# Kernel optimization log

Hardware: AMD Instinct MI355X
Metric: run time of the kernel (lower is better)

Reference implementation:

```python
import jax, jax.numpy as jnp
import numpy as np

F_IN, F_OUT, H, L_ENC, L_DEC, HORIZON = 32, 8, 64, 2, 2, 48
B, T = 2048, 512


def _lstm_cell(x, h, c, Wih, Whh, bih, bhh):
    # PyTorch LSTMCell: gates ordered i, f, g, o
    g = x @ Wih.T + bih + h @ Whh.T + bhh
    i, f, gg, o = jnp.split(g, 4, axis=-1)
    c_new = jax.nn.sigmoid(f) * c + jax.nn.sigmoid(i) * jnp.tanh(gg)
    h_new = jax.nn.sigmoid(o) * jnp.tanh(c_new)
    return h_new, c_new


def setup_inputs() -> dict:
    key = jax.random.key(0)
    ks = jax.random.split(key, 16)
    s = 1.0 / np.sqrt(H)
    u = lambda k, shape: jax.random.uniform(k, shape, jnp.float32, -s, s)
    return {
        "X": jax.random.normal(ks[0], (B, T, F_IN), jnp.float32),
        "X_mask": jnp.ones((B, T, F_IN), jnp.float32),
        "W_emb": u(ks[1], (H, F_IN)),
        "b_emb": u(ks[2], (H,)),
        "enc_Wih": u(ks[3], (L_ENC, 4 * H, H)),
        "enc_Whh": u(ks[4], (L_ENC, 4 * H, H)),
        "enc_bih": u(ks[5], (L_ENC, 4 * H)),
        "enc_bhh": u(ks[6], (L_ENC, 4 * H)),
        "dec_Wih": u(ks[7], (L_DEC, 4 * H, H)),
        "dec_Whh": u(ks[8], (L_DEC, 4 * H, H)),
        "dec_bih": u(ks[9], (L_DEC, 4 * H)),
        "dec_bhh": u(ks[10], (L_DEC, 4 * H)),
        "W_reg": u(ks[11], (F_OUT, H)),
        "b_reg": u(ks[12], (F_OUT,)),
    }


def reference(X, X_mask, W_emb, b_emb, enc_Wih, enc_Whh, enc_bih, enc_bhh,
              dec_Wih, dec_Whh, dec_bih, dec_bhh, W_reg, b_reg):
    batch = X.shape[0]
    # Token embedding for all timesteps at once: [T, B, H]
    emb = jnp.einsum('btf,hf->tbh', X, W_emb) + b_emb

    h0 = jnp.zeros((L_ENC, batch, H), X.dtype)
    c0 = jnp.zeros((L_ENC, batch, H), X.dtype)

    def enc_step(carry, x_t):
        h, c = carry
        h_t = x_t
        hs, cs = [], []
        for i in range(L_ENC):
            h_t, c_t = _lstm_cell(h_t, h[i], c[i], enc_Wih[i], enc_Whh[i], enc_bih[i], enc_bhh[i])
            hs.append(h_t)
            cs.append(c_t)
        return (jnp.stack(hs), jnp.stack(cs)), None

    (h_enc, _), _ = jax.lax.scan(enc_step, (h0, c0), emb)

    # Decoder: hidden states initialized from encoder h, cells from zero
    c_dec0 = jnp.zeros((L_DEC, batch, H), X.dtype)

    def dec_step(carry, _):
        h, c = carry
        h_t = h[-1]
        hs, cs = [], []
        for i in range(L_DEC):
            h_t, c_t = _lstm_cell(h_t, h[i], c[i], dec_Wih[i], dec_Whh[i], dec_bih[i], dec_bhh[i])
            hs.append(h_t)
            cs.append(c_t)
        y_t = h_t @ W_reg.T + b_reg
        return (jnp.stack(hs), jnp.stack(cs)), y_t

    _, ys = jax.lax.scan(dec_step, (h_enc, c_dec0), None, length=HORIZON)
    return jnp.transpose(ys, (1, 0, 2))  # [B, horizon, F_OUT]
```

## Files before the change

kernel.cpp:

```cpp
#include <hip/hip_runtime.h>
#include <hip/hip_bf16.h>

typedef __bf16 bf16x8 __attribute__((ext_vector_type(8)));
typedef float  f32x4  __attribute__((ext_vector_type(4)));

#define MFMA16(a,b,c) __builtin_amdgcn_mfma_f32_16x16x32_bf16((a),(b),(c),0,0,0)

__device__ __forceinline__ bf16x8 cvt8(f32x4 a, f32x4 b){
  bf16x8 r;
  r[0]=(__bf16)a[0]; r[1]=(__bf16)a[1]; r[2]=(__bf16)a[2]; r[3]=(__bf16)a[3];
  r[4]=(__bf16)b[0]; r[5]=(__bf16)b[1]; r[6]=(__bf16)b[2]; r[7]=(__bf16)b[3];
  return r;
}
__device__ __forceinline__ bf16x8 ld8(const float* p){
  return cvt8(*(const f32x4*)p, *(const f32x4*)(p+4));
}
__device__ __forceinline__ float sigm(float x){
  return __builtin_amdgcn_rcpf(1.f + __expf(-x));
}
__device__ __forceinline__ float tanhx(float x){
  return 1.f - 2.f*__builtin_amdgcn_rcpf(1.f + __expf(2.f*x));
}
__device__ __forceinline__ f32x4 sp(float v){ return (f32x4){v,v,v,v}; }

__device__ __forceinline__ float dppx8(float v){
  return __int_as_float(__builtin_amdgcn_update_dpp(
      0, __float_as_int(v), 0x128, 0xF, 0xF, true));
}
__device__ __forceinline__ float swz4(float v){
  return __int_as_float(__builtin_amdgcn_ds_swizzle(__float_as_int(v), 0x101F));
}

extern "C" __global__ void __launch_bounds__(1024, 4)
seq2seq_kernel(const float* __restrict__ X,
               const float* __restrict__ Wemb, const float* __restrict__ bemb,
               const float* __restrict__ eWih, const float* __restrict__ eWhh,
               const float* __restrict__ ebih, const float* __restrict__ ebhh,
               const float* __restrict__ dWih, const float* __restrict__ dWhh,
               const float* __restrict__ dbih, const float* __restrict__ dbhh,
               const float* __restrict__ Wreg, const float* __restrict__ breg,
               float* __restrict__ out)
{
  __shared__ __align__(16) __bf16 XA[2][8][136];
  __shared__ __align__(16) __bf16 H1s[2][8][72];

  const int tid  = (int)threadIdx.x;
  const int w    = tid >> 6;
  const int grp  = w >> 3;
  const bool g0  = (grp == 0);
  const int wt   = w & 7;
  const int lane = tid & 63;
  const int col  = lane & 15;
  const int quad = lane >> 4;
  const int row8 = col & 7;
  const int b0   = (int)blockIdx.x * 8;
  const int brow = b0 + row8;

  const bool hib = (col & 8) != 0;
  const bool qhb = (quad & 2) != 0;
  const int  ewr = 4*(quad & 1) + (hib ? 1 : 0) + (qhb ? 2 : 0);
  const int  ewu = 8*wt + (col & 7);

  for (int i = tid; i < 2*8*136; i += 1024) (&XA[0][0][0])[i]  = (__bf16)0.f;
  for (int i = tid; i < 2*8*72;  i += 1024) (&H1s[0][0][0])[i] = (__bf16)0.f;

  bf16x8 wf[8];
  float  gb[2];
#pragma unroll
  for (int ti=0; ti<2; ++ti){
    const int n = 64*(2*ti + (col>>3)) + 8*wt + (col&7);
    gb[ti] = ebih[grp*256+n] + ebhh[grp*256+n];
#pragma unroll
    for (int ks=0; ks<4; ++ks){
      const float* srcw = (ks < 2) ? eWih : eWhh;
      wf[ti*4+ks] = ld8(srcw + ((size_t)(grp*256+n))*64 + (ks&1)*32 + quad*8);
    }
  }

  const int ue = (w&3)*16 + col;
  bf16x8 wembf;
  float eb = 0.f;
  const float* xb = X + (size_t)brow*512*32 + quad*8;
  f32x4 pa0, pb0, pa1, pb1;
  if (w < 4){
    wembf = ld8(Wemb + ue*32 + quad*8);
    eb = bemb[ue];
    pa1 = *(const f32x4*)(xb+32); pb1 = *(const f32x4*)(xb+36);
    pa0 = *(const f32x4*)(xb+64); pb0 = *(const f32x4*)(xb+68);
  }

  float cC = 0.f;

  auto EWF = [&](f32x4 A0, f32x4 A1, float& c) -> float {
    float lo0 = qhb ? A0[2] : A0[0];
    float hi0 = qhb ? A0[3] : A0[1];
    float lo1 = qhb ? A1[2] : A1[0];
    float hi1 = qhb ? A1[3] : A1[1];
    float a0s = hib ? hi0 : lo0, a0x = hib ? lo0 : hi0;
    float a1s = hib ? hi1 : lo1, a1x = hib ? lo1 : hi1;
    float r0 = dppx8(a0x), r1 = dppx8(a1x);
    float gi = hib ? r0  : a0s;
    float gf = hib ? a0s : r0;
    float gg = hib ? r1  : a1s;
    float go = hib ? a1s : r1;
    float i0 = sigm(gi), f0 = sigm(gf), gt = tanhx(gg), o0 = sigm(go);
    c = f0*c + i0*gt;
    return o0*tanhx(c);
  };

  auto FUSED0 = [&](const int I){
    const int Px = (I+1)&1, Pr = I&1;
    bf16x8 ax0 = *(const bf16x8*)&XA[Px][row8][ 0 + quad*8];
    bf16x8 ax1 = *(const bf16x8*)&XA[Px][row8][32 + quad*8];
    bf16x8 ah0 = *(const bf16x8*)&XA[Pr][row8][64 + quad*8];
    bf16x8 ah1 = *(const bf16x8*)&XA[Pr][row8][96 + quad*8];
    f32x4 A0 = sp(gb[0]), A1 = sp(gb[1]);
    A0=MFMA16(ax0,wf[0],A0); A1=MFMA16(ax0,wf[4],A1);
    A0=MFMA16(ax1,wf[1],A0); A1=MFMA16(ax1,wf[5],A1);
    A0=MFMA16(ah0,wf[2],A0); A1=MFMA16(ah0,wf[6],A1);
    A0=MFMA16(ah1,wf[3],A0); A1=MFMA16(ah1,wf[7],A1);
    if (I < 510 && w < 4){
      const int s = I&1;
      f32x4 xr0 = s ? pa1 : pa0, xr1 = s ? pb1 : pb0;
      f32x4 ea = MFMA16(cvt8(xr0,xr1), wembf, sp(eb));
      int tn = I+4; if (tn > 511) tn = 511;
      f32x4 na = *(const f32x4*)(xb + (size_t)tn*32);
      f32x4 nb = *(const f32x4*)(xb + (size_t)tn*32 + 4);
      if (s){ pa1=na; pb1=nb; } else { pa0=na; pb0=nb; }
      if (quad < 2){
#pragma unroll
        for (int r=0; r<4; ++r) XA[s][quad*4+r][ue] = (__bf16)ea[r];
      }
    }
    XA[Px][ewr][64+ewu] = (__bf16)EWF(A0, A1, cC);
  };

  auto FUSED1 = [&](const int I){
    const int Px = (I+1)&1, Pr = I&1;
    bf16x8 ah0 = *(const bf16x8*)&XA[Pr][row8][64 + quad*8];
    bf16x8 ah1 = *(const bf16x8*)&XA[Pr][row8][96 + quad*8];
    bf16x8 ag0 = *(const bf16x8*)&H1s[Px][row8][ 0 + quad*8];
    bf16x8 ag1 = *(const bf16x8*)&H1s[Px][row8][32 + quad*8];
    f32x4 A0 = sp(gb[0]), A1 = sp(gb[1]);
    A0=MFMA16(ah0,wf[0],A0); A1=MFMA16(ah0,wf[4],A1);
    A0=MFMA16(ah1,wf[1],A0); A1=MFMA16(ah1,wf[5],A1);
    A0=MFMA16(ag0,wf[2],A0); A1=MFMA16(ag0,wf[6],A1);
    A0=MFMA16(ag1,wf[3],A0); A1=MFMA16(ag1,wf[7],A1);
    H1s[Pr][ewr][ewu] = (__bf16)EWF(A0, A1, cC);
  };

  __syncthreads();

  if (w < 4){
    f32x4 x0a = *(const f32x4*)xb, x0b = *(const f32x4*)(xb+4);
    f32x4 e0 = MFMA16(cvt8(x0a,x0b), wembf, sp(eb));
    if (quad < 2){
#pragma unroll
      for (int r=0; r<4; ++r) XA[0][quad*4+r][ue] = (__bf16)e0[r];
    }
  }
  __syncthreads();
  if (g0) FUSED0(-1);
  __syncthreads();

#define SLOT(I) { if (g0) FUSED0(I); else FUSED1(I); __syncthreads(); }
  for (int ii=0; ii<255; ++ii){
    SLOT(2*ii)
    SLOT(2*ii+1)
  }
  SLOT(510)
#undef SLOT

  if (!g0) FUSED1(511);
  __syncthreads();

  for (int idx = tid; idx < 8*64; idx += 1024){
    XA[1][idx>>6][idx&63] = H1s[1][idx>>6][idx&63];
  }
  bf16x8 wr0 = ld8(Wreg + (col&7)*64 +  0 + quad*8);
  bf16x8 wr1 = ld8(Wreg + (col&7)*64 + 32 + quad*8);
  const float rb = breg[col&7];
  float gbd[2];
#pragma unroll
  for (int l=0; l<2; ++l){
    const int n = 64*(col>>2) + 4*w + (col&3);
    gbd[l] = dbih[l*256+n] + dbhh[l*256+n];
#pragma unroll
    for (int ks=0; ks<4; ++ks){
      const float* srcw = (ks < 2) ? dWih : dWhh;
      wf[l*4+ks] = ld8(srcw + ((size_t)(l*256+n))*64 + (ks&1)*32 + quad*8);
    }
  }
  const int  gated = col >> 2;
  const bool b0d = (gated & 1) != 0;
  const bool b1d = (gated & 2) != 0;
  const int  rd  = 4*(quad & 1) + (b1d ? 1 : 0) + (qhb ? 2 : 0);
  const int  udj = 4*w + (col & 3);
  float cD0 = 0.f, cD1 = 0.f;
  __syncthreads();

  auto EWD = [&](f32x4 B, float& c) -> float {
    float lo  = qhb ? B[2] : B[0];
    float hi2 = qhb ? B[3] : B[1];
    float a  = b1d ? hi2 : lo;
    float ax = b1d ? lo  : hi2;
    float pA = swz4(a);
    float pB = swz4(ax);
    float qA = dppx8(ax);
    float qB = dppx8(pB);
    float gi = b1d ? (b0d?qB:qA) : (b0d?pA:a);
    float gf = b1d ? (b0d?qA:qB) : (b0d?a:pA);
    float gg = b1d ? (b0d?pA:a) : (b0d?qB:qA);
    float go = b1d ? (b0d?a:pA) : (b0d?qA:qB);
    float i0 = sigm(gi), f0 = sigm(gf), gt = tanhx(gg), o0 = sigm(go);
    c = f0*c + i0*gt;
    return o0*tanhx(c);
  };

  auto Ystore = [&](const int t){
    const int hp = t&1;
    f32x4 ya = sp(rb);
    bf16x8 y0 = *(const bf16x8*)&H1s[hp][row8][ 0 + quad*8];
    bf16x8 y1 = *(const bf16x8*)&H1s[hp][row8][32 + quad*8];
    ya = MFMA16(y0, wr0, ya);
    ya = MFMA16(y1, wr1, ya);
    if (quad < 2 && col < 8){
#pragma unroll
      for (int r=0; r<4; ++r)
        out[((size_t)(b0 + quad*4 + r)*48 + t)*8 + col] = ya[r];
    }
  };

#define DSTEP(T) {                                                         \
    const int P = (T)&1, Pm = P^1;                                         \
    {                                                                      \
      bf16x8 ax0 = *(const bf16x8*)&XA[Pm][row8][ 0 + quad*8];             \
      bf16x8 ax1 = *(const bf16x8*)&XA[Pm][row8][32 + quad*8];             \
      bf16x8 ah0 = *(const bf16x8*)&XA[Pm][row8][64 + quad*8];             \
      bf16x8 ah1 = *(const bf16x8*)&XA[Pm][row8][96 + quad*8];             \
      f32x4 B0 = sp(gbd[0]);                                               \
      B0=MFMA16(ax0,wf[0],B0); B0=MFMA16(ax1,wf[1],B0);                    \
      B0=MFMA16(ah0,wf[2],B0); B0=MFMA16(ah1,wf[3],B0);                    \
      float h = EWD(B0, cD0);                                              \
      if (!b0d) XA[P][rd][64+udj] = (__bf16)h;                             \
      if ((T) && w == 0) Ystore((T)-1);                                    \
    }                                                                      \
    __syncthreads();                                                       \
    {                                                                      \
      bf16x8 ah0 = *(const bf16x8*)&XA[P][row8][64 + quad*8];              \
      bf16x8 ah1 = *(const bf16x8*)&XA[P][row8][96 + quad*8];              \
      bf16x8 ag0 = *(const bf16x8*)&H1s[Pm][row8][ 0 + quad*8];            \
      bf16x8 ag1 = *(const bf16x8*)&H1s[Pm][row8][32 + quad*8];            \
      f32x4 B1 = sp(gbd[1]);                                               \
      B1=MFMA16(ah0,wf[4],B1); B1=MFMA16(ah1,wf[5],B1);                    \
      B1=MFMA16(ag0,wf[6],B1); B1=MFMA16(ag1,wf[7],B1);                    \
      float h = EWD(B1, cD1);                                              \
      if (!b0d){ H1s[P][rd][udj] = (__bf16)h; XA[P][rd][udj] = (__bf16)h; }\
    }                                                                      \
    __syncthreads();                                                       \
  }

  for (int tt=0; tt<24; ++tt){
    DSTEP(2*tt)
    DSTEP(2*tt+1)
  }
#undef DSTEP
  if (w == 0) Ystore(47);
}

extern "C" void kernel_launch(void* const* d_in, const int* in_sizes, int n_in,
                              void* d_out, int out_size, void* d_ws, size_t ws_size,
                              hipStream_t stream)
{
  (void)in_sizes; (void)n_in; (void)out_size; (void)d_ws; (void)ws_size;
  const float* X    = (const float*)d_in[0];
  const float* Wemb = (const float*)d_in[2];
  const float* bemb = (const float*)d_in[3];
  const float* eWih = (const float*)d_in[4];
  const float* eWhh = (const float*)d_in[5];
  const float* ebih = (const float*)d_in[6];
  const float* ebhh = (const float*)d_in[7];
  const float* dWih = (const float*)d_in[8];
  const float* dWhh = (const float*)d_in[9];
  const float* dbih = (const float*)d_in[10];
  const float* dbhh = (const float*)d_in[11];
  const float* Wreg = (const float*)d_in[12];
  const float* breg = (const float*)d_in[13];
  float* out = (float*)d_out;

  seq2seq_kernel<<<dim3(256), dim3(1024), 0, stream>>>(
      X, Wemb, bemb, eWih, eWhh, ebih, ebhh,
      dWih, dWhh, dbih, dbhh, Wreg, breg, out);
}
```

Before: 607.8 us.

## Split encoder slots into GEMM/EW phases and XOR-swizzle LDS layout

The encoder step for each layer is split into a GEMM phase and an elementwise phase, with a barrier between them. Layer 0's GEMM now runs while layer 1 does its elementwise work, and the reverse, so MFMA and VALU work from the two wave groups can overlap within the CU. The padded shared-memory rows are replaced by an XOR swizzle on 8-element chunks to avoid bank conflicts without the padding. The cost is twice as many block-wide barriers per encoder timestep, which lengthens the serial recurrence chain.

```diff
diff --git a/kernel.cpp b/kernel.cpp
--- a/kernel.cpp
+++ b/kernel.cpp
@@ -41,8 +41,8 @@
                const float* __restrict__ Wreg, const float* __restrict__ breg,
                float* __restrict__ out)
 {
-  __shared__ __align__(16) __bf16 XA[2][8][136];
-  __shared__ __align__(16) __bf16 H1s[2][8][72];
+  __shared__ __align__(16) __bf16 XA[2][8][128];
+  __shared__ __align__(16) __bf16 H1s[2][8][64];
 
   const int tid  = (int)threadIdx.x;
   const int w    = tid >> 6;
@@ -61,8 +61,15 @@
   const int  ewr = 4*(quad & 1) + (hib ? 1 : 0) + (qhb ? 2 : 0);
   const int  ewu = 8*wt + (col & 7);
 
-  for (int i = tid; i < 2*8*136; i += 1024) (&XA[0][0][0])[i]  = (__bf16)0.f;
-  for (int i = tid; i < 2*8*72;  i += 1024) (&H1s[0][0][0])[i] = (__bf16)0.f;
+  const int rx  = row8 * 128;
+  const int rh  = row8 * 64;
+  const int gA0 = ((quad    ) ^ row8) * 8;
+  const int gA1 = ((quad + 4) ^ row8) * 8;
+  const int sw0 = ewr*128 + 64 + ((wt ^ ewr) << 3) + (ewu & 7);
+  const int sw1 = ewr*64       + ((wt ^ ewr) << 3) + (ewu & 7);
+
+  for (int i = tid; i < 2*8*128; i += 1024) (&XA[0][0][0])[i]  = (__bf16)0.f;
+  for (int i = tid; i < 2*8*64;  i += 1024) (&H1s[0][0][0])[i] = (__bf16)0.f;
 
   bf16x8 wf[8];
   float  gb[2];
@@ -77,7 +84,8 @@
     }
   }
 
-  const int ue = (w&3)*16 + col;
+  const int ue  = (w&3)*16 + col;
+  const int gue = ue >> 3, oue = ue & 7;
   bf16x8 wembf;
   float eb = 0.f;
   const float* xb = X + (size_t)brow*512*32 + quad*8;
@@ -90,12 +98,13 @@
   }
 
   float cC = 0.f;
-
-  auto EWF = [&](f32x4 A0, f32x4 A1, float& c) -> float {
-    float lo0 = qhb ? A0[2] : A0[0];
-    float hi0 = qhb ? A0[3] : A0[1];
-    float lo1 = qhb ? A1[2] : A1[0];
-    float hi1 = qhb ? A1[3] : A1[1];
+  f32x4 A0h, A1h;
+
+  auto EWF = [&](float& c) -> float {
+    float lo0 = qhb ? A0h[2] : A0h[0];
+    float hi0 = qhb ? A0h[3] : A0h[1];
+    float lo1 = qhb ? A1h[2] : A1h[0];
+    float hi1 = qhb ? A1h[3] : A1h[1];
     float a0s = hib ? hi0 : lo0, a0x = hib ? lo0 : hi0;
     float a1s = hib ? hi1 : lo1, a1x = hib ? lo1 : hi1;
     float r0 = dppx8(a0x), r1 = dppx8(a1x);
@@ -108,12 +117,14 @@
     return o0*tanhx(c);
   };
 
-  auto FUSED0 = [&](const int I){
+  auto GEMM0R = [&](const int I){
     const int Px = (I+1)&1, Pr = I&1;
-    bf16x8 ax0 = *(const bf16x8*)&XA[Px][row8][ 0 + quad*8];
-    bf16x8 ax1 = *(const bf16x8*)&XA[Px][row8][32 + quad*8];
-    bf16x8 ah0 = *(const bf16x8*)&XA[Pr][row8][64 + quad*8];
-    bf16x8 ah1 = *(const bf16x8*)&XA[Pr][row8][96 + quad*8];
+    const __bf16* xbuf = &XA[Px][0][0];
+    const __bf16* hbuf = &XA[Pr][0][0];
+    bf16x8 ax0 = *(const bf16x8*)(xbuf + rx + gA0);
+    bf16x8 ax1 = *(const bf16x8*)(xbuf + rx + gA1);
+    bf16x8 ah0 = *(const bf16x8*)(hbuf + rx + 64 + gA0);
+    bf16x8 ah1 = *(const bf16x8*)(hbuf + rx + 64 + gA1);
     f32x4 A0 = sp(gb[0]), A1 = sp(gb[1]);
     A0=MFMA16(ax0,wf[0],A0); A1=MFMA16(ax0,wf[4],A1);
     A0=MFMA16(ax1,wf[1],A0); A1=MFMA16(ax1,wf[5],A1);
@@ -129,24 +140,37 @@
       if (s){ pa1=na; pb1=nb; } else { pa0=na; pb0=nb; }
       if (quad < 2){
 #pragma unroll
-        for (int r=0; r<4; ++r) XA[s][quad*4+r][ue] = (__bf16)ea[r];
+        for (int r=0; r<4; ++r){
+          const int rr = quad*4 + r;
+          XA[s][rr][((gue ^ rr) << 3) | oue] = (__bf16)ea[r];
+        }
       }
     }
-    XA[Px][ewr][64+ewu] = (__bf16)EWF(A0, A1, cC);
-  };
-
-  auto FUSED1 = [&](const int I){
-    const int Px = (I+1)&1, Pr = I&1;
-    bf16x8 ah0 = *(const bf16x8*)&XA[Pr][row8][64 + quad*8];
-    bf16x8 ah1 = *(const bf16x8*)&XA[Pr][row8][96 + quad*8];
-    bf16x8 ag0 = *(const bf16x8*)&H1s[Px][row8][ 0 + quad*8];
-    bf16x8 ag1 = *(const bf16x8*)&H1s[Px][row8][32 + quad*8];
+    A0h = A0; A1h = A1;
+  };
+
+  auto EW0S = [&](const int I){
+    (&XA[(I+1)&1][0][0])[sw0] = (__bf16)EWF(cC);
+  };
+
+  auto GEMM1R = [&](const int I){
+    const int Pr = I&1, Ph = (I+1)&1;
+    const __bf16* hbuf = &XA[Pr][0][0];
+    const __bf16* gbuf = &H1s[Ph][0][0];
+    bf16x8 ah0 = *(const bf16x8*)(hbuf + rx + 64 + gA0);
+    bf16x8 ah1 = *(const bf16x8*)(hbuf + rx + 64 + gA1);
+    bf16x8 ag0 = *(const bf16x8*)(gbuf + rh + gA0);
+    bf16x8 ag1 = *(const bf16x8*)(gbuf + rh + gA1);
     f32x4 A0 = sp(gb[0]), A1 = sp(gb[1]);
     A0=MFMA16(ah0,wf[0],A0); A1=MFMA16(ah0,wf[4],A1);
     A0=MFMA16(ah1,wf[1],A0); A1=MFMA16(ah1,wf[5],A1);
     A0=MFMA16(ag0,wf[2],A0); A1=MFMA16(ag0,wf[6],A1);
     A0=MFMA16(ag1,wf[3],A0); A1=MFMA16(ag1,wf[7],A1);
-    H1s[Pr][ewr][ewu] = (__bf16)EWF(A0, A1, cC);
+    A0h = A0; A1h = A1;
+  };
+
+  auto EW1S = [&](const int I){
+    (&H1s[I&1][0][0])[sw1] = (__bf16)EWF(cC);
   };
 
   __syncthreads();
@@ -156,22 +180,34 @@
     f32x4 e0 = MFMA16(cvt8(x0a,x0b), wembf, sp(eb));
     if (quad < 2){
 #pragma unroll
-      for (int r=0; r<4; ++r) XA[0][quad*4+r][ue] = (__bf16)e0[r];
-    }
-  }
-  __syncthreads();
-  if (g0) FUSED0(-1);
-  __syncthreads();
-
-#define SLOT(I) { if (g0) FUSED0(I); else FUSED1(I); __syncthreads(); }
-  for (int ii=0; ii<255; ++ii){
-    SLOT(2*ii)
-    SLOT(2*ii+1)
-  }
-  SLOT(510)
-#undef SLOT
-
-  if (!g0) FUSED1(511);
+      for (int r=0; r<4; ++r){
+        const int rr = quad*4 + r;
+        XA[0][rr][((gue ^ rr) << 3) | oue] = (__bf16)e0[r];
+      }
+    }
+  }
+  __syncthreads();
+  if (g0) GEMM0R(-1);
+  __syncthreads();
+  if (g0) EW0S(-1);
+  __syncthreads();
+
+  if (g0) GEMM0R(0);
+  __syncthreads();
+  if (g0) EW0S(0); else GEMM1R(0);
+  __syncthreads();
+  for (int I=1; I<511; ++I){
+    if (g0) GEMM0R(I); else EW1S(I-1);
+    __syncthreads();
+    if (g0) EW0S(I); else GEMM1R(I);
+    __syncthreads();
+  }
+
+  if (!g0) EW1S(510);
+  __syncthreads();
+  if (!g0) GEMM1R(511);
+  __syncthreads();
+  if (!g0) EW1S(511);
   __syncthreads();
 
   for (int idx = tid; idx < 8*64; idx += 1024){
@@ -196,6 +232,10 @@
   const bool b1d = (gated & 2) != 0;
   const int  rd  = 4*(quad & 1) + (b1d ? 1 : 0) + (qhb ? 2 : 0);
   const int  udj = 4*w + (col & 3);
+  const int  gdd = udj >> 3;
+  const int  swdx = rd*128 + 64 + ((gdd ^ rd) << 3) + (udj & 7);
+  const int  swdh = rd*64       + ((gdd ^ rd) << 3) + (udj & 7);
+  const int  swdi = rd*128      + ((gdd ^ rd) << 3) + (udj & 7);
   float cD0 = 0.f, cD1 = 0.f;
   __syncthreads();
 
@@ -219,9 +259,10 @@
 
   auto Ystore = [&](const int t){
     const int hp = t&1;
+    const __bf16* hb_ = &H1s[hp][0][0];
     f32x4 ya = sp(rb);
-    bf16x8 y0 = *(const bf16x8*)&H1s[hp][row8][ 0 + quad*8];
-    bf16x8 y1 = *(const bf16x8*)&H1s[hp][row8][32 + quad*8];
+    bf16x8 y0 = *(const bf16x8*)(hb_ + rh + gA0);
+    bf16x8 y1 = *(const bf16x8*)(hb_ + rh + gA1);
     ya = MFMA16(y0, wr0, ya);
     ya = MFMA16(y1, wr1, ya);
     if (quad < 2 && col < 8){
@@ -234,28 +275,32 @@
 #define DSTEP(T) {                                                         \
     const int P = (T)&1, Pm = P^1;                                         \
     {                                                                      \
-      bf16x8 ax0 = *(const bf16x8*)&XA[Pm][row8][ 0 + quad*8];             \
-      bf16x8 ax1 = *(const bf16x8*)&XA[Pm][row8][32 + quad*8];             \
-      bf16x8 ah0 = *(const bf16x8*)&XA[Pm][row8][64 + quad*8];             \
-      bf16x8 ah1 = *(const bf16x8*)&XA[Pm][row8][96 + quad*8];             \
+      const __bf16* xb_ = &XA[Pm][0][0];                                   \
+      bf16x8 ax0 = *(const bf16x8*)(xb_ + rx + gA0);                       \
+      bf16x8 ax1 = *(const bf16x8*)(xb_ + rx + gA1);                       \
+      bf16x8 ah0 = *(const bf16x8*)(xb_ + rx + 64 + gA0);                  \
+      bf16x8 ah1 = *(const bf16x8*)(xb_ + rx + 64 + gA1);                  \
       f32x4 B0 = sp(gbd[0]);                                               \
       B0=MFMA16(ax0,wf[0],B0); B0=MFMA16(ax1,wf[1],B0);                    \
       B0=MFMA16(ah0,wf[2],B0); B0=MFMA16(ah1,wf[3],B0);                    \
       float h = EWD(B0, cD0);                                              \
-      if (!b0d) XA[P][rd][64+udj] = (__bf16)h;                             \
+      if (!b0d) (&XA[P][0][0])[swdx] = (__bf16)h;                          \
       if ((T) && w == 0) Ystore((T)-1);                                    \
     }                                                                      \
     __syncthreads();                                                       \
     {                                                                      \
-      bf16x8 ah0 = *(const bf16x8*)&XA[P][row8][64 + quad*8];              \
-      bf16x8 ah1 = *(const bf16x8*)&XA[P][row8][96 + quad*8];              \
-      bf16x8 ag0 = *(const bf16x8*)&H1s[Pm][row8][ 0 + quad*8];            \
-      bf16x8 ag1 = *(const bf16x8*)&H1s[Pm][row8][32 + quad*8];            \
+      const __bf16* xb_ = &XA[P][0][0];                                    \
+      const __bf16* hb_ = &H1s[Pm][0][0];                                  \
+      bf16x8 ah0 = *(const bf16x8*)(xb_ + rx + 64 + gA0);                  \
+      bf16x8 ah1 = *(const bf16x8*)(xb_ + rx + 64 + gA1);                  \
+      bf16x8 ag0 = *(const bf16x8*)(hb_ + rh + gA0);                       \
+      bf16x8 ag1 = *(const bf16x8*)(hb_ + rh + gA1);                       \
       f32x4 B1 = sp(gbd[1]);                                               \
       B1=MFMA16(ah0,wf[4],B1); B1=MFMA16(ah1,wf[5],B1);                    \
       B1=MFMA16(ag0,wf[6],B1); B1=MFMA16(ag1,wf[7],B1);                    \
       float h = EWD(B1, cD1);                                              \
-      if (!b0d){ H1s[P][rd][udj] = (__bf16)h; XA[P][rd][udj] = (__bf16)h; }\
+      if (!b0d){ (&H1s[P][0][0])[swdh] = (__bf16)h;                        \
+                 (&XA[P][0][0])[swdi]  = (__bf16)h; }                      \
     }                                                                      \
     __syncthreads();                                                       \
   }
```

New measurement: 906.5 us. +49.2%, slower.

## Fold embedding into layer-0 input weights and fuse gate activations via exp2

Applied to the files above, without the earlier changes.

Precomputes W_ih0·W_emb (and the embedding bias) into the layer-0 encoder weights, so each step runs one MFMA directly on raw X instead of a separate embedding MFMA plus an LDS round trip. Gate weights and biases are pre-scaled by log2(e) (2·log2(e) for the g gate) so the LSTM elementwise stage uses exp2 directly and combines reciprocals (fewer rcp ops per cell). The x prefetch distance shrinks accordingly and the initial embedding pass and one barrier are removed. Clamps are added to keep exp2 finite; the folded weights are rounded to bf16 after the product, which slightly changes numerics.

```diff
diff --git a/kernel.cpp b/kernel.cpp
--- a/kernel.cpp
+++ b/kernel.cpp
@@ -5,6 +5,16 @@
 typedef float  f32x4  __attribute__((ext_vector_type(4)));
 
 #define MFMA16(a,b,c) __builtin_amdgcn_mfma_f32_16x16x32_bf16((a),(b),(c),0,0,0)
+
+#if __has_builtin(__builtin_amdgcn_exp2f)
+#define EXP2(x) __builtin_amdgcn_exp2f(x)
+#else
+#define EXP2(x) exp2f(x)
+#endif
+#define RCP(x) __builtin_amdgcn_rcpf(x)
+
+#define KL  1.44269504088896340736f
+#define K2L 2.88539008177792681472f
 
 __device__ __forceinline__ bf16x8 cvt8(f32x4 a, f32x4 b){
   bf16x8 r;
@@ -12,16 +22,29 @@
   r[4]=(__bf16)b[0]; r[5]=(__bf16)b[1]; r[6]=(__bf16)b[2]; r[7]=(__bf16)b[3];
   return r;
 }
+__device__ __forceinline__ f32x4 sp(float v){ return (f32x4){v,v,v,v}; }
 __device__ __forceinline__ bf16x8 ld8(const float* p){
   return cvt8(*(const f32x4*)p, *(const f32x4*)(p+4));
 }
-__device__ __forceinline__ float sigm(float x){
-  return __builtin_amdgcn_rcpf(1.f + __expf(-x));
-}
-__device__ __forceinline__ float tanhx(float x){
-  return 1.f - 2.f*__builtin_amdgcn_rcpf(1.f + __expf(2.f*x));
-}
-__device__ __forceinline__ f32x4 sp(float v){ return (f32x4){v,v,v,v}; }
+__device__ __forceinline__ bf16x8 ld8s(const float* p, float s){
+  f32x4 a = *(const f32x4*)p, b = *(const f32x4*)(p+4);
+  return cvt8(a*sp(s), b*sp(s));
+}
+
+__device__ __forceinline__ float lstm_ew(float gi, float gf, float gg,
+                                         float go, float& c){
+  float Ef = EXP2(-gf);
+  float Ei = EXP2(-gi);
+  float gc = fminf(fmaxf(gg, -60.f), 60.f);
+  float G  = EXP2(gc);
+  float Rf = RCP(1.f + Ef);
+  float Rig= RCP((1.f + Ei) * (1.f + G));
+  c = c*Rf + (G - 1.f)*Rig;
+  float Eo = EXP2(-go);
+  float ch = fminf(fmaxf(c, -30.f), 30.f);
+  float C2 = EXP2(ch * K2L);
+  return (C2 - 1.f) * RCP((1.f + Eo) * (1.f + C2));
+}
 
 __device__ __forceinline__ float dppx8(float v){
   return __int_as_float(__builtin_amdgcn_update_dpp(
@@ -68,25 +91,39 @@
   float  gb[2];
 #pragma unroll
   for (int ti=0; ti<2; ++ti){
-    const int n = 64*(2*ti + (col>>3)) + 8*wt + (col&7);
-    gb[ti] = ebih[grp*256+n] + ebhh[grp*256+n];
-#pragma unroll
-    for (int ks=0; ks<4; ++ks){
-      const float* srcw = (ks < 2) ? eWih : eWhh;
-      wf[ti*4+ks] = ld8(srcw + ((size_t)(grp*256+n))*64 + (ks&1)*32 + quad*8);
+    const int gate = 2*ti + (col>>3);
+    const int n = 64*gate + 8*wt + (col&7);
+    const float sc = (gate == 2) ? K2L : KL;
+    if (g0){
+      f32x4 acL = sp(0.f), acH = sp(0.f);
+      float bx = 0.f;
+      const float* wr_ = eWih + (size_t)n*64;
+      for (int k=0; k<64; ++k){
+        float a = wr_[k];
+        bx += a * bemb[k];
+        f32x4 m0 = *(const f32x4*)(Wemb + k*32 + quad*8);
+        f32x4 m1 = *(const f32x4*)(Wemb + k*32 + quad*8 + 4);
+        acL += sp(a)*m0; acH += sp(a)*m1;
+      }
+      wf[ti*4+0] = cvt8(acL*sp(sc), acH*sp(sc));
+      wf[ti*4+2] = ld8s(eWhh + (size_t)n*64 +      quad*8, sc);
+      wf[ti*4+3] = ld8s(eWhh + (size_t)n*64 + 32 + quad*8, sc);
+      gb[ti] = (ebih[n] + ebhh[n] + bx) * sc;
+    } else {
+      const int m = 256 + n;
+      wf[ti*4+0] = ld8s(eWih + (size_t)m*64 +      quad*8, sc);
+      wf[ti*4+1] = ld8s(eWih + (size_t)m*64 + 32 + quad*8, sc);
+      wf[ti*4+2] = ld8s(eWhh + (size_t)m*64 +      quad*8, sc);
+      wf[ti*4+3] = ld8s(eWhh + (size_t)m*64 + 32 + quad*8, sc);
+      gb[ti] = (ebih[m] + ebhh[m]) * sc;
     }
   }
 
-  const int ue = (w&3)*16 + col;
-  bf16x8 wembf;
-  float eb = 0.f;
   const float* xb = X + (size_t)brow*512*32 + quad*8;
   f32x4 pa0, pb0, pa1, pb1;
-  if (w < 4){
-    wembf = ld8(Wemb + ue*32 + quad*8);
-    eb = bemb[ue];
-    pa1 = *(const f32x4*)(xb+32); pb1 = *(const f32x4*)(xb+36);
-    pa0 = *(const f32x4*)(xb+64); pb0 = *(const f32x4*)(xb+68);
+  if (g0){
+    pa0 = *(const f32x4*)(xb);     pb0 = *(const f32x4*)(xb+4);
+    pa1 = *(const f32x4*)(xb+32);  pb1 = *(const f32x4*)(xb+36);
   }
 
   float cC = 0.f;
@@ -103,35 +140,25 @@
     float gf = hib ? a0s : r0;
     float gg = hib ? r1  : a1s;
     float go = hib ? a1s : r1;
-    float i0 = sigm(gi), f0 = sigm(gf), gt = tanhx(gg), o0 = sigm(go);
-    c = f0*c + i0*gt;
-    return o0*tanhx(c);
+    return lstm_ew(gi, gf, gg, go, c);
   };
 
   auto FUSED0 = [&](const int I){
     const int Px = (I+1)&1, Pr = I&1;
-    bf16x8 ax0 = *(const bf16x8*)&XA[Px][row8][ 0 + quad*8];
-    bf16x8 ax1 = *(const bf16x8*)&XA[Px][row8][32 + quad*8];
+    f32x4 xr0 = Px ? pa1 : pa0, xr1 = Px ? pb1 : pb0;
+    bf16x8 axf = cvt8(xr0, xr1);
+    {
+      int tn = I+3; if (tn > 511) tn = 511;
+      f32x4 na = *(const f32x4*)(xb + (size_t)tn*32);
+      f32x4 nb = *(const f32x4*)(xb + (size_t)tn*32 + 4);
+      if (Px){ pa1=na; pb1=nb; } else { pa0=na; pb0=nb; }
+    }
     bf16x8 ah0 = *(const bf16x8*)&XA[Pr][row8][64 + quad*8];
     bf16x8 ah1 = *(const bf16x8*)&XA[Pr][row8][96 + quad*8];
     f32x4 A0 = sp(gb[0]), A1 = sp(gb[1]);
-    A0=MFMA16(ax0,wf[0],A0); A1=MFMA16(ax0,wf[4],A1);
-    A0=MFMA16(ax1,wf[1],A0); A1=MFMA16(ax1,wf[5],A1);
+    A0=MFMA16(axf,wf[0],A0); A1=MFMA16(axf,wf[4],A1);
     A0=MFMA16(ah0,wf[2],A0); A1=MFMA16(ah0,wf[6],A1);
     A0=MFMA16(ah1,wf[3],A0); A1=MFMA16(ah1,wf[7],A1);
-    if (I < 510 && w < 4){
-      const int s = I&1;
-      f32x4 xr0 = s ? pa1 : pa0, xr1 = s ? pb1 : pb0;
-      f32x4 ea = MFMA16(cvt8(xr0,xr1), wembf, sp(eb));
-      int tn = I+4; if (tn > 511) tn = 511;
-      f32x4 na = *(const f32x4*)(xb + (size_t)tn*32);
-      f32x4 nb = *(const f32x4*)(xb + (size_t)tn*32 + 4);
-      if (s){ pa1=na; pb1=nb; } else { pa0=na; pb0=nb; }
-      if (quad < 2){
-#pragma unroll
-        for (int r=0; r<4; ++r) XA[s][quad*4+r][ue] = (__bf16)ea[r];
-      }
-    }
     XA[Px][ewr][64+ewu] = (__bf16)EWF(A0, A1, cC);
   };
 
@@ -139,7 +166,7 @@
     const int Px = (I+1)&1, Pr = I&1;
     bf16x8 ah0 = *(const bf16x8*)&XA[Pr][row8][64 + quad*8];
     bf16x8 ah1 = *(const bf16x8*)&XA[Pr][row8][96 + quad*8];
-    bf16x8 ag0 = *(const bf16x8*)&H1s[Px][row8][ 0 + quad*8];
+    bf16x8 ag0 = *(const bf16x8*)&H1s[Px][row8][quad*8];
     bf16x8 ag1 = *(const bf16x8*)&H1s[Px][row8][32 + quad*8];
     f32x4 A0 = sp(gb[0]), A1 = sp(gb[1]);
     A0=MFMA16(ah0,wf[0],A0); A1=MFMA16(ah0,wf[4],A1);
@@ -151,15 +178,6 @@
 
   __syncthreads();
 
-  if (w < 4){
-    f32x4 x0a = *(const f32x4*)xb, x0b = *(const f32x4*)(xb+4);
-    f32x4 e0 = MFMA16(cvt8(x0a,x0b), wembf, sp(eb));
-    if (quad < 2){
-#pragma unroll
-      for (int r=0; r<4; ++r) XA[0][quad*4+r][ue] = (__bf16)e0[r];
-    }
-  }
-  __syncthreads();
   if (g0) FUSED0(-1);
   __syncthreads();
 
@@ -180,18 +198,19 @@
   bf16x8 wr0 = ld8(Wreg + (col&7)*64 +  0 + quad*8);
   bf16x8 wr1 = ld8(Wreg + (col&7)*64 + 32 + quad*8);
   const float rb = breg[col&7];
+  const int  gated = col >> 2;
+  const float scd = (gated == 2) ? K2L : KL;
   float gbd[2];
 #pragma unroll
   for (int l=0; l<2; ++l){
-    const int n = 64*(col>>2) + 4*w + (col&3);
-    gbd[l] = dbih[l*256+n] + dbhh[l*256+n];
+    const int n = 64*gated + 4*w + (col&3);
+    gbd[l] = (dbih[l*256+n] + dbhh[l*256+n]) * scd;
 #pragma unroll
     for (int ks=0; ks<4; ++ks){
       const float* srcw = (ks < 2) ? dWih : dWhh;
-      wf[l*4+ks] = ld8(srcw + ((size_t)(l*256+n))*64 + (ks&1)*32 + quad*8);
+      wf[l*4+ks] = ld8s(srcw + ((size_t)(l*256+n))*64 + (ks&1)*32 + quad*8, scd);
     }
   }
-  const int  gated = col >> 2;
   const bool b0d = (gated & 1) != 0;
   const bool b1d = (gated & 2) != 0;
   const int  rd  = 4*(quad & 1) + (b1d ? 1 : 0) + (qhb ? 2 : 0);
@@ -212,15 +231,13 @@
     float gf = b1d ? (b0d?qA:qB) : (b0d?a:pA);
     float gg = b1d ? (b0d?pA:a) : (b0d?qB:qA);
     float go = b1d ? (b0d?a:pA) : (b0d?qA:qB);
-    float i0 = sigm(gi), f0 = sigm(gf), gt = tanhx(gg), o0 = sigm(go);
-    c = f0*c + i0*gt;
-    return o0*tanhx(c);
+    return lstm_ew(gi, gf, gg, go, c);
   };
 
   auto Ystore = [&](const int t){
     const int hp = t&1;
     f32x4 ya = sp(rb);
-    bf16x8 y0 = *(const bf16x8*)&H1s[hp][row8][ 0 + quad*8];
+    bf16x8 y0 = *(const bf16x8*)&H1s[hp][row8][quad*8];
     bf16x8 y1 = *(const bf16x8*)&H1s[hp][row8][32 + quad*8];
     ya = MFMA16(y0, wr0, ya);
     ya = MFMA16(y1, wr1, ya);
```

Measured after the change: 829.2 us. 1.36x slower.
